# Kernel optimization log

Hardware: AMD Instinct MI355X
Metric: run time of the kernel (lower is better)

## Reference

```python
import jax, jax.numpy as jnp
import numpy as np

NUM_CLASSES = 21
THRESH = 0.5
NEGPOS = 3
VAR0, VAR1 = 0.1, 0.2
FEAT = 19
N_ANCH = 9
B = 256
NUM_OBJS = 12
P = FEAT * FEAT * N_ANCH  # 3249


def make_priors():
    # 19x19 grid, 3 scales x 3 aspect ratios (1, 2, 1/2) -> 9 anchors/cell, center form
    cxy = (np.arange(FEAT, dtype=np.float32) + 0.5) / FEAT
    cx, cy = np.meshgrid(cxy, cxy, indexing='ij')  # [19,19]
    scales = np.array([0.1, 0.2, 0.35], dtype=np.float32)
    ratios = np.array([1.0, 2.0, 0.5], dtype=np.float32)
    w = (scales[:, None] * np.sqrt(ratios)[None, :]).reshape(-1)  # [9]
    h = (scales[:, None] / np.sqrt(ratios)[None, :]).reshape(-1)
    cx = np.broadcast_to(cx[:, :, None], (FEAT, FEAT, N_ANCH))
    cy = np.broadcast_to(cy[:, :, None], (FEAT, FEAT, N_ANCH))
    w = np.broadcast_to(w[None, None, :], (FEAT, FEAT, N_ANCH))
    h = np.broadcast_to(h[None, None, :], (FEAT, FEAT, N_ANCH))
    pri = np.stack([cx, cy, w, h], axis=-1).reshape(-1, 4)
    return jnp.asarray(np.clip(pri, 1e-3, 1.0))


def setup_inputs() -> dict:
    key = jax.random.key(0)
    k1, k2, k3, k4, k5 = jax.random.split(key, 5)
    loc_data = jax.random.normal(k1, (B, P, 4), dtype=jnp.float32)
    conf_data = jax.random.normal(k2, (B, P, NUM_CLASSES), dtype=jnp.float32)
    priors = make_priors()
    xy = jax.random.uniform(k3, (B, NUM_OBJS, 2), minval=0.05, maxval=0.65)
    wh = jax.random.uniform(k4, (B, NUM_OBJS, 2), minval=0.05, maxval=0.30)
    labels = jax.random.randint(k5, (B, NUM_OBJS), 0, NUM_CLASSES - 1).astype(jnp.float32)
    targets = jnp.concatenate([xy, xy + wh, labels[..., None]], axis=-1)  # [B,O,5]
    return {"loc_data": loc_data, "conf_data": conf_data, "priors": priors, "targets": targets}


def point_form(boxes):  # (cx,cy,w,h) -> (x1,y1,x2,y2)
    return jnp.concatenate([boxes[:, :2] - boxes[:, 2:] / 2,
                            boxes[:, :2] + boxes[:, 2:] / 2], axis=1)


def jaccard(a, b):  # a: [n,4], b: [m,4] point form -> [n,m]
    lt = jnp.maximum(a[:, None, :2], b[None, :, :2])
    rb = jnp.minimum(a[:, None, 2:], b[None, :, 2:])
    inter = jnp.prod(jnp.clip(rb - lt, 0.0, None), axis=-1)
    area_a = jnp.prod(a[:, 2:] - a[:, :2], axis=-1)
    area_b = jnp.prod(b[:, 2:] - b[:, :2], axis=-1)
    return inter / (area_a[:, None] + area_b[None, :] - inter)


def encode(matched, priors):  # matched point-form [P,4], priors center-form [P,4]
    g_cxcy = ((matched[:, :2] + matched[:, 2:]) / 2 - priors[:, :2]) / (VAR0 * priors[:, 2:])
    g_wh = jnp.log((matched[:, 2:] - matched[:, :2]) / priors[:, 2:]) / VAR1
    return jnp.concatenate([g_cxcy, g_wh], axis=1)


def match_one(truths, labels, priors, priors_pt):
    overlaps = jaccard(truths, priors_pt)          # [O,P]
    best_prior_idx = jnp.argmax(overlaps, axis=1)  # [O]
    best_truth_ov = jnp.max(overlaps, axis=0)      # [P]
    best_truth_idx = jnp.argmax(overlaps, axis=0)  # [P]
    best_truth_ov = best_truth_ov.at[best_prior_idx].set(2.0)
    best_truth_idx = best_truth_idx.at[best_prior_idx].set(jnp.arange(truths.shape[0]))
    matches = truths[best_truth_idx]               # [P,4]
    conf = labels[best_truth_idx] + 1
    conf = jnp.where(best_truth_ov < THRESH, 0, conf)
    return encode(matches, priors), conf


def reference(loc_data, conf_data, priors, targets):
    truths = targets[:, :, :4]
    labels = targets[:, :, 4].astype(jnp.int32)
    priors_pt = point_form(priors)
    loc_t, conf_t = jax.vmap(lambda t, l: match_one(t, l, priors, priors_pt))(truths, labels)
    loc_t = jax.lax.stop_gradient(loc_t)
    conf_t = jax.lax.stop_gradient(conf_t)

    pos = conf_t > 0                                               # [B,P]
    # smooth L1 (sum) over matched priors
    d = loc_data - loc_t
    ad = jnp.abs(d)
    sl1 = jnp.where(ad < 1.0, 0.5 * d * d, ad - 0.5)
    loss_l = jnp.sum(sl1 * pos[..., None].astype(sl1.dtype))

    # per-prior CE = logsumexp - logit[target]
    lse = jax.nn.logsumexp(conf_data, axis=-1)                     # [B,P]
    gathered = jnp.take_along_axis(conf_data, conf_t[..., None], axis=2)[..., 0]
    ce = lse - gathered                                            # [B,P]

    # hard negative mining: double argsort rank of neg losses
    loss_c_mine = jnp.where(pos, 0.0, ce)
    loss_idx = jnp.argsort(-loss_c_mine, axis=1)
    idx_rank = jnp.argsort(loss_idx, axis=1)
    num_pos = jnp.sum(pos, axis=1, keepdims=True)                  # [B,1]
    num_neg = jnp.minimum(NEGPOS * num_pos, P - 1)
    neg = idx_rank < num_neg

    sel = pos | neg
    loss_c = jnp.sum(jnp.where(sel, ce, 0.0))

    have_centerloss = jnp.max(sel.reshape(B, FEAT, FEAT, N_ANCH), axis=3).reshape(-1)
    conf_t_featuremap = jnp.max(conf_t.reshape(B, FEAT, FEAT, N_ANCH), axis=3).reshape(-1)

    N = jnp.sum(num_pos).astype(loc_data.dtype)
    return loss_l / N, loss_c / N, conf_t_featuremap, have_centerloss
```

## Files before the change

### kernel.cpp

```cpp
#include <hip/hip_runtime.h>
#include <math.h>

#pragma clang fp contract(off)

#define BB      256
#define PP      3249
#define NCLS    21
#define NOBJ    12
#define CELLS   361
#define THRESH_ 0.5f
#define HB      4096

typedef float vf4 __attribute__((ext_vector_type(4), aligned(4)));


struct Row { vf4 a, b, c, d, e; float f; };

__device__ __forceinline__ Row load_row(const float* cd) {
    const vf4* q = (const vf4*)cd;
    Row r;
    r.a = q[0]; r.b = q[1]; r.c = q[2]; r.d = q[3]; r.e = q[4];
    r.f = cd[20];
    return r;
}

__device__ __forceinline__ float lse21(const Row& r) {
    float m = r.a[0];
    m = fmaxf(m, r.a[1]); m = fmaxf(m, r.a[2]); m = fmaxf(m, r.a[3]);
    m = fmaxf(m, r.b[0]); m = fmaxf(m, r.b[1]); m = fmaxf(m, r.b[2]); m = fmaxf(m, r.b[3]);
    m = fmaxf(m, r.c[0]); m = fmaxf(m, r.c[1]); m = fmaxf(m, r.c[2]); m = fmaxf(m, r.c[3]);
    m = fmaxf(m, r.d[0]); m = fmaxf(m, r.d[1]); m = fmaxf(m, r.d[2]); m = fmaxf(m, r.d[3]);
    m = fmaxf(m, r.e[0]); m = fmaxf(m, r.e[1]); m = fmaxf(m, r.e[2]); m = fmaxf(m, r.e[3]);
    m = fmaxf(m, r.f);
    float s = 0.0f;
    s += expf(r.a[0]-m); s += expf(r.a[1]-m); s += expf(r.a[2]-m); s += expf(r.a[3]-m);
    s += expf(r.b[0]-m); s += expf(r.b[1]-m); s += expf(r.b[2]-m); s += expf(r.b[3]-m);
    s += expf(r.c[0]-m); s += expf(r.c[1]-m); s += expf(r.c[2]-m); s += expf(r.c[3]-m);
    s += expf(r.d[0]-m); s += expf(r.d[1]-m); s += expf(r.d[2]-m); s += expf(r.d[3]-m);
    s += expf(r.e[0]-m); s += expf(r.e[1]-m); s += expf(r.e[2]-m); s += expf(r.e[3]-m);
    s += expf(r.f-m);
    return logf(s) + m;
}

template <int NBITS>
__device__ __forceinline__ void scan_hist(const unsigned* key_arr, int* hist,
                                          unsigned prefix, unsigned pmask,
                                          int shift, int tid, int lane) {
    for (int i = tid; i < PP; i += 1024) {
        unsigned key = key_arr[i];
        bool active = ((key & pmask) == prefix);
        unsigned bin = (key >> shift) & ((1u << NBITS) - 1u);
        unsigned long long mm = __ballot(active);
#pragma unroll
        for (int bit = 0; bit < NBITS; ++bit) {
            unsigned long long bb = __ballot(active && ((bin >> bit) & 1));
            mm &= ((bin >> bit) & 1) ? bb : ~bb;
        }
        if (active && (__ffsll((unsigned long long)mm) - 1 == lane))
            atomicAdd(&hist[bin], (int)__popcll(mm));
    }
}

__device__ __forceinline__ void pick_bin(const int* hist, int nbins, int kv, int lane,
                                         int* s_chosen, int* s_knext, int* s_cnt) {
    const int per = nbins >> 6;
    const int base = lane * per;
    int ls = 0;
    for (int k = 0; k < per; ++k) ls += hist[base + k];
    int x = ls;
#pragma unroll
    for (int off = 1; off < 64; off <<= 1) {
        int y = __shfl_down(x, off);
        if (lane + off < 64) x += y;
    }
    int cum = x - ls;
    for (int k = per - 1; k >= 0; --k) {
        int h = hist[base + k];
        if (cum < kv && kv <= cum + h) { *s_chosen = base + k; *s_knext = kv - cum; *s_cnt = h; }
        cum += h;
    }
}

__global__ __launch_bounds__(1024, 4) void fused_kernel(
    const float* __restrict__ loc, const float* __restrict__ conf,
    const float* __restrict__ priors, const float* __restrict__ targets,
    int* __restrict__ numpos, double* __restrict__ lossl,
    double* __restrict__ lossc, float* __restrict__ out)
{
    const int b = blockIdx.x, tid = threadIdx.x;
    const int lane = tid & 63, wid = tid >> 6;

    __shared__ float s_tx1[NOBJ], s_ty1[NOBJ], s_tx2[NOBJ], s_ty2[NOBJ];
    __shared__ float s_area_t[NOBJ];
    __shared__ int   s_label[NOBJ];
    __shared__ float s_bov[PP];
    __shared__ short s_bidx[PP];
    __shared__ float s_lse[PP];
    __shared__ float s_c0[PP];
    __shared__ unsigned s_key[PP];
    __shared__ unsigned char s_ct[PP];
    __shared__ int   s_bpi[NOBJ];
    __shared__ float s_wov[NOBJ][16];
    __shared__ int   s_widx[NOBJ][16];
    __shared__ int s_hist[2][HB];
    __shared__ int s_chosen, s_knext, s_cnt, s_nneg;
    __shared__ unsigned s_f;
    __shared__ double s_pl[16];
    __shared__ int    s_pn[16];
    __shared__ double s_pc[16];

    if (tid < NOBJ) {
        const float* t = targets + ((size_t)b * NOBJ + tid) * 5;
        float x1 = t[0], y1 = t[1], x2 = t[2], y2 = t[3];
        s_tx1[tid] = x1; s_ty1[tid] = y1; s_tx2[tid] = x2; s_ty2[tid] = y2;
        s_label[tid] = (int)t[4];
        s_area_t[tid] = (x2 - x1) * (y2 - y1);
    }
    __syncthreads();

    const float* confb = conf + (size_t)b * PP * NCLS;
    const int p0 = tid, p1 = tid + 1024, p2 = tid + 2048, p3 = tid + 3072;
    const bool h3 = (p3 < PP);

    vf4 pr0 = *(const vf4*)(priors + 4 * p0);
    vf4 pr1 = *(const vf4*)(priors + 4 * p1);
    vf4 pr2 = *(const vf4*)(priors + 4 * p2);
    vf4 pr3; if (h3) pr3 = *(const vf4*)(priors + 4 * p3);
    Row ra = load_row(confb + (size_t)p0 * NCLS);

    float l_bov[NOBJ];
    int   l_bidx[NOBJ];
#pragma unroll
    for (int j = 0; j < NOBJ; ++j) { l_bov[j] = -1.0f; l_bidx[j] = 0x7FFFFFFF; }

    auto iou_body = [&](vf4 prr, int p) {
        float cx = prr[0], cy = prr[1], w = prr[2], h = prr[3];
        float px1 = cx - w / 2.0f, py1 = cy - h / 2.0f;
        float px2 = cx + w / 2.0f, py2 = cy + h / 2.0f;
        float area_p = (px2 - px1) * (py2 - py1);
        float bov = -1.0f; int bidx = 0;
#pragma unroll
        for (int j = 0; j < NOBJ; ++j) {
            float ltx = fmaxf(s_tx1[j], px1);
            float lty = fmaxf(s_ty1[j], py1);
            float rbx = fminf(s_tx2[j], px2);
            float rby = fminf(s_ty2[j], py2);
            float iw = fmaxf(rbx - ltx, 0.0f);
            float ih = fmaxf(rby - lty, 0.0f);
            float inter = iw * ih;
            float iou = inter / ((s_area_t[j] + area_p) - inter);
            if (iou > bov) { bov = iou; bidx = j; }
            if (iou > l_bov[j]) { l_bov[j] = iou; l_bidx[j] = p; }
        }
        s_bov[p] = bov;
        s_bidx[p] = (short)bidx;
    };
    iou_body(pr0, p0);
    iou_body(pr1, p1);
    iou_body(pr2, p2);
    if (h3) iou_body(pr3, p3);

#pragma unroll
    for (int j = 0; j < NOBJ; ++j) {
        float ov = l_bov[j]; int ix = l_bidx[j];
#pragma unroll
        for (int off = 32; off > 0; off >>= 1) {
            float ov2 = __shfl_xor(ov, off);
            int   ix2 = __shfl_xor(ix, off);
            if (ov2 > ov || (ov2 == ov && ix2 < ix)) { ov = ov2; ix = ix2; }
        }
        if (lane == 0) { s_wov[j][wid] = ov; s_widx[j][wid] = ix; }
    }

    {
        Row rb = load_row(confb + (size_t)p1 * NCLS);
        s_lse[p0] = lse21(ra); s_c0[p0] = ra.a[0];
        Row rc = load_row(confb + (size_t)p2 * NCLS);
        s_lse[p1] = lse21(rb); s_c0[p1] = rb.a[0];
        Row rd; if (h3) rd = load_row(confb + (size_t)p3 * NCLS);
        s_lse[p2] = lse21(rc); s_c0[p2] = rc.a[0];
        if (h3) { s_lse[p3] = lse21(rd); s_c0[p3] = rd.a[0]; }
    }
    __syncthreads();

    if (tid < NOBJ) {
        float ov = s_wov[tid][0]; int ix = s_widx[tid][0];
#pragma unroll
        for (int w2 = 1; w2 < 16; ++w2) {
            float ov2 = s_wov[tid][w2]; int ix2 = s_widx[tid][w2];
            if (ov2 > ov || (ov2 == ov && ix2 < ix)) { ov = ov2; ix = ix2; }
        }
        s_bpi[tid] = ix;
    }
    __syncthreads();

    int bpi[NOBJ];
#pragma unroll
    for (int j = 0; j < NOBJ; ++j) bpi[j] = s_bpi[j];

    int my_pos = 0;
    double my_lossl = 0.0;
    for (int p = tid; p < PP; p += 1024) {
        int jov = -1;
#pragma unroll
        for (int j = 0; j < NOBJ; ++j) if (bpi[j] == p) jov = j;
        int idx; float ov;
        if (jov >= 0) { idx = jov; ov = 2.0f; }
        else          { idx = (int)s_bidx[p]; ov = s_bov[p]; }
        int c = (ov < THRESH_) ? 0 : (s_label[idx] + 1);
        s_ct[p] = (unsigned char)c;

        float lse = s_lse[p];
        float cdc = (c == 0) ? s_c0[p] : confb[(size_t)p * NCLS + c];
        float ce  = lse - cdc;

        float v = (c > 0) ? 0.0f : ce;
        s_key[p] = __float_as_uint(v);
        s_bov[p] = ce;

        if (c > 0) {
            ++my_pos;
            float cx = priors[4*p+0], cy = priors[4*p+1], w = priors[4*p+2], h = priors[4*p+3];
            float m0 = s_tx1[idx], m1 = s_ty1[idx], m2 = s_tx2[idx], m3 = s_ty2[idx];
            float g0 = ((m0 + m2) / 2.0f - cx) / (0.1f * w);
            float g1 = ((m1 + m3) / 2.0f - cy) / (0.1f * h);
            float g2 = logf((m2 - m0) / w) / 0.2f;
            float g3 = logf((m3 - m1) / h) / 0.2f;
            const float* ld = loc + ((size_t)b * PP + p) * 4;
            float d0 = ld[0] - g0, d1 = ld[1] - g1, d2 = ld[2] - g2, d3 = ld[3] - g3;
            float a0 = fabsf(d0), a1 = fabsf(d1), a2 = fabsf(d2), a3 = fabsf(d3);
            my_lossl += (double)((a0 < 1.0f) ? 0.5f * d0 * d0 : a0 - 0.5f);
            my_lossl += (double)((a1 < 1.0f) ? 0.5f * d1 * d1 : a1 - 0.5f);
            my_lossl += (double)((a2 < 1.0f) ? 0.5f * d2 * d2 : a2 - 0.5f);
            my_lossl += (double)((a3 < 1.0f) ? 0.5f * d3 * d3 : a3 - 0.5f);
        }
    }
#pragma unroll
    for (int off = 32; off > 0; off >>= 1) {
        my_lossl += __shfl_down(my_lossl, off);
        my_pos   += __shfl_down(my_pos, off);
    }
    if (lane == 0) { s_pl[wid] = my_lossl; s_pn[wid] = my_pos; }
    for (int k = tid; k < 2 * HB; k += 1024) ((int*)s_hist)[k] = 0;
    __syncthreads();

    unsigned prefix = 0u, pmask = 0u, fstar = 0u;
    int ptie = 0x7FFFFFFF;
    bool resolved = false;

    if (tid == 0) {
        double L = 0.0; int n = 0;
#pragma unroll
        for (int w2 = 0; w2 < 16; ++w2) { L += s_pl[w2]; n += s_pn[w2]; }
        lossl[b] = L; numpos[b] = n;
        s_nneg = min(3 * n, PP - 1);
    }
    scan_hist<12>(s_key, s_hist[0], 0u, 0u, 20, tid, lane);
    __syncthreads();
    if (tid < 64) pick_bin(s_hist[0], HB, s_nneg, lane, &s_chosen, &s_knext, &s_cnt);
    else { for (int k = tid - 64; k < HB; k += 960) s_hist[1][k] = 0; }
    __syncthreads();
    prefix = ((unsigned)s_chosen) << 20; pmask = 0xFFF00000u;
    if (s_cnt == 1) {
        for (int i = tid; i < PP; i += 1024) {
            unsigned key = s_key[i];
            if ((key & pmask) == prefix) s_f = key;
        }
        __syncthreads();
        fstar = s_f; resolved = true;
    }

    if (!resolved) {
        scan_hist<12>(s_key, s_hist[1], prefix, pmask, 8, tid, lane);
        __syncthreads();
        if (tid < 64) pick_bin(s_hist[1], HB, s_knext, lane, &s_chosen, &s_knext, &s_cnt);
        else { for (int k = tid - 64; k < HB; k += 960) s_hist[0][k] = 0; }
        __syncthreads();
        prefix |= ((unsigned)s_chosen) << 8; pmask |= 0x000FFF00u;
        if (s_cnt == 1) {
            for (int i = tid; i < PP; i += 1024) {
                unsigned key = s_key[i];
                if ((key & pmask) == prefix) s_f = key;
            }
            __syncthreads();
            fstar = s_f; resolved = true;
        }
    }

    if (!resolved) {
        scan_hist<8>(s_key, s_hist[0], prefix, pmask, 0, tid, lane);
        __syncthreads();
        if (tid < 64) pick_bin(s_hist[0], 256, s_knext, lane, &s_chosen, &s_knext, &s_cnt);
        else { for (int k = tid - 64; k < HB; k += 960) s_hist[1][k] = 0; }
        __syncthreads();
        prefix |= (unsigned)s_chosen;
        fstar = prefix;
        if (s_knext < s_cnt) {
            int* hist = s_hist[1];
            for (int i = tid; i < PP; i += 1024) {
                bool active = (s_key[i] == fstar);
                unsigned bin = 4095u - (unsigned)i;
                unsigned long long mm = __ballot(active);
#pragma unroll
                for (int bit = 0; bit < 12; ++bit) {
                    unsigned long long bb = __ballot(active && ((bin >> bit) & 1));
                    mm &= ((bin >> bit) & 1) ? bb : ~bb;
                }
                if (active && (__ffsll((unsigned long long)mm) - 1 == lane))
                    atomicAdd(&hist[bin], (int)__popcll(mm));
            }
            __syncthreads();
            if (tid < 64) pick_bin(hist, HB, s_knext, lane, &s_chosen, &s_knext, &s_cnt);
            __syncthreads();
            ptie = 4095 - s_chosen;
        }
    }

    double my_c = 0.0;
    for (int cI = tid; cI < CELLS; cI += 1024) {
        int mc = 0, hv = 0;
#pragma unroll
        for (int a = 0; a < 9; ++a) {
            int p = cI * 9 + a;
            int cv = s_ct[p];
            unsigned v = s_key[p];
            bool sel = (cv > 0) || (v > fstar) || (v == fstar && p <= ptie);
            mc = (cv > mc) ? cv : mc;
            hv |= sel ? 1 : 0;
            if (sel) my_c += (double)s_bov[p];
        }
        out[2 + (size_t)b * CELLS + cI] = (float)mc;
        out[2 + (size_t)BB * CELLS + (size_t)b * CELLS + cI] = (float)hv;
    }

#pragma unroll
    for (int off = 32; off > 0; off >>= 1) my_c += __shfl_down(my_c, off);
    if (lane == 0) s_pc[wid] = my_c;
    __syncthreads();
    if (tid == 0) {
        double L = 0.0;
#pragma unroll
        for (int w2 = 0; w2 < 16; ++w2) L += s_pc[w2];
        lossc[b] = L;
    }
}

__global__ __launch_bounds__(256) void finalize_kernel(
    const int* __restrict__ numpos, const double* __restrict__ lossl,
    const double* __restrict__ lossc, float* __restrict__ out)
{
    __shared__ double s_l[256], s_c[256];
    __shared__ int s_n[256];
    int tid = threadIdx.x;
    s_n[tid] = numpos[tid];
    s_l[tid] = lossl[tid];
    s_c[tid] = lossc[tid];
    __syncthreads();
    for (int s = 128; s > 0; s >>= 1) {
        if (tid < s) { s_n[tid] += s_n[tid + s]; s_l[tid] += s_l[tid + s]; s_c[tid] += s_c[tid + s]; }
        __syncthreads();
    }
    if (tid == 0) {
        double N = (double)s_n[0];
        out[0] = (float)(s_l[0] / N);
        out[1] = (float)(s_c[0] / N);
    }
}

extern "C" void kernel_launch(void* const* d_in, const int* in_sizes, int n_in,
                              void* d_out, int out_size, void* d_ws, size_t ws_size,
                              hipStream_t stream) {
    const float* loc     = (const float*)d_in[0];
    const float* conf    = (const float*)d_in[1];
    const float* priors  = (const float*)d_in[2];
    const float* targets = (const float*)d_in[3];
    float* out = (float*)d_out;

    double* ws_lossl  = (double*)d_ws;
    double* ws_lossc  = ws_lossl + BB;
    int*    ws_numpos = (int*)(ws_lossc + BB);

    hipLaunchKernelGGL(fused_kernel, dim3(BB), dim3(1024), 0, stream,
                       loc, conf, priors, targets, ws_numpos, ws_lossl, ws_lossc, out);
    hipLaunchKernelGGL(finalize_kernel, dim3(1), dim3(256), 0, stream,
                       ws_numpos, ws_lossl, ws_lossc, out);
}
```

Before: 141.9 us.

## Split IoU/logsumexp into a wide prep kernel and use 8-bit radix select

Moves the per-prior IoU matching and logsumexp over the 21 class logits into a separate prep kernel launched over 13 chunks per batch. This gives the memory-heavy conf read many more, smaller blocks than the original 256 large blocks. Per-object best-prior results are packed into 64-bit keys (IoU, inverted index) and reduced across chunks in the select kernel. The hard-negative radix select changes from 12-bit histograms (4096 bins) to four 8-bit passes plus a two-level tie-break, which shrinks the shared-memory footprint. The cost is an extra launch and a round trip of the per-prior records through global memory.

Measured after the change: 142.7 us. About the same (+0.5%).

```diff
diff --git a/kernel.cpp b/kernel.cpp
--- a/kernel.cpp
+++ b/kernel.cpp
@@ -8,10 +8,11 @@
 #define NCLS    21
 #define NOBJ    12
 #define CELLS   361
+#define CH      13
 #define THRESH_ 0.5f
-#define HB      4096
 
 typedef float vf4 __attribute__((ext_vector_type(4), aligned(4)));
+typedef float vrec __attribute__((ext_vector_type(4)));
 
 
 struct Row { vf4 a, b, c, d, e; float f; };
@@ -43,30 +44,24 @@
 }
 
 template <int NBITS>
-__device__ __forceinline__ void scan_hist(const unsigned* key_arr, int* hist,
-                                          unsigned prefix, unsigned pmask,
-                                          int shift, int tid, int lane) {
-    for (int i = tid; i < PP; i += 1024) {
-        unsigned key = key_arr[i];
-        bool active = ((key & pmask) == prefix);
-        unsigned bin = (key >> shift) & ((1u << NBITS) - 1u);
-        unsigned long long mm = __ballot(active);
-#pragma unroll
-        for (int bit = 0; bit < NBITS; ++bit) {
-            unsigned long long bb = __ballot(active && ((bin >> bit) & 1));
-            mm &= ((bin >> bit) & 1) ? bb : ~bb;
-        }
-        if (active && (__ffsll((unsigned long long)mm) - 1 == lane))
-            atomicAdd(&hist[bin], (int)__popcll(mm));
-    }
+__device__ __forceinline__ void agg_add(int* hist, bool active, unsigned bin, int lane) {
+    unsigned long long mm = __ballot(active);
+#pragma unroll
+    for (int bit = 0; bit < NBITS; ++bit) {
+        unsigned long long bb = __ballot(active && ((bin >> bit) & 1));
+        mm &= ((bin >> bit) & 1) ? bb : ~bb;
+    }
+    if (active && (__ffsll(mm) - 1 == lane))
+        atomicAdd(&hist[bin], (int)__popcll(mm));
 }
 
 __device__ __forceinline__ void pick_bin(const int* hist, int nbins, int kv, int lane,
                                          int* s_chosen, int* s_knext, int* s_cnt) {
-    const int per = nbins >> 6;
+    const int per = (nbins >= 64) ? (nbins >> 6) : 1;
     const int base = lane * per;
     int ls = 0;
-    for (int k = 0; k < per; ++k) ls += hist[base + k];
+    if (base < nbins)
+        for (int k = 0; k < per; ++k) ls += hist[base + k];
     int x = ls;
 #pragma unroll
     for (int off = 1; off < 64; off <<= 1) {
@@ -74,16 +69,85 @@
         if (lane + off < 64) x += y;
     }
     int cum = x - ls;
-    for (int k = per - 1; k >= 0; --k) {
-        int h = hist[base + k];
-        if (cum < kv && kv <= cum + h) { *s_chosen = base + k; *s_knext = kv - cum; *s_cnt = h; }
-        cum += h;
-    }
-}
-
-__global__ __launch_bounds__(1024, 4) void fused_kernel(
+    if (base < nbins) {
+        for (int k = per - 1; k >= 0; --k) {
+            int h = hist[base + k];
+            if (cum < kv && kv <= cum + h) { *s_chosen = base + k; *s_knext = kv - cum; *s_cnt = h; }
+            cum += h;
+        }
+    }
+}
+
+__global__ __launch_bounds__(256, 6) void prep_kernel(
+    const float* __restrict__ conf, const float* __restrict__ priors,
+    const float* __restrict__ targets, vrec* __restrict__ recs,
+    unsigned long long* __restrict__ pt)
+{
+    const int chunk = blockIdx.x, b = blockIdx.y;
+    const int tid = threadIdx.x, lane = tid & 63, wid = tid >> 6;
+    const int p = chunk * 256 + tid;
+    const bool valid = (p < PP);
+
+    __shared__ float s_tx1[NOBJ], s_ty1[NOBJ], s_tx2[NOBJ], s_ty2[NOBJ], s_area[NOBJ];
+    __shared__ unsigned long long s_wk[NOBJ][4];
+
+    if (tid < NOBJ) {
+        const float* t = targets + ((size_t)b * NOBJ + tid) * 5;
+        float x1 = t[0], y1 = t[1], x2 = t[2], y2 = t[3];
+        s_tx1[tid] = x1; s_ty1[tid] = y1; s_tx2[tid] = x2; s_ty2[tid] = y2;
+        s_area[tid] = (x2 - x1) * (y2 - y1);
+    }
+    __syncthreads();
+
+    vf4 pr = {0.0f, 0.0f, 0.0f, 0.0f};
+    if (valid) pr = *(const vf4*)(priors + 4 * p);
+    float px1 = pr[0] - pr[2] / 2.0f, py1 = pr[1] - pr[3] / 2.0f;
+    float px2 = pr[0] + pr[2] / 2.0f, py2 = pr[1] + pr[3] / 2.0f;
+    float area_p = (px2 - px1) * (py2 - py1);
+
+    float bov = -1.0f; int bidx = 0;
+#pragma unroll
+    for (int j = 0; j < NOBJ; ++j) {
+        float ltx = fmaxf(s_tx1[j], px1);
+        float lty = fmaxf(s_ty1[j], py1);
+        float rbx = fminf(s_tx2[j], px2);
+        float rby = fminf(s_ty2[j], py2);
+        float iw = fmaxf(rbx - ltx, 0.0f);
+        float ih = fmaxf(rby - lty, 0.0f);
+        float inter = iw * ih;
+        float iou = inter / ((s_area[j] + area_p) - inter);
+        if (iou > bov) { bov = iou; bidx = j; }
+        unsigned long long k = valid
+            ? (((unsigned long long)__float_as_uint(iou) << 32) | (0xFFFFFFFFu - (unsigned)p))
+            : 0ull;
+#pragma unroll
+        for (int off = 32; off > 0; off >>= 1) {
+            unsigned long long k2 = __shfl_xor(k, off);
+            if (k2 > k) k = k2;
+        }
+        if (lane == 0) s_wk[j][wid] = k;
+    }
+
+    if (valid) {
+        Row r = load_row(conf + ((size_t)b * PP + p) * NCLS);
+        float lse = lse21(r);
+        vrec rec;
+        rec[0] = bov; rec[1] = __int_as_float(bidx); rec[2] = lse; rec[3] = r.a[0];
+        recs[(size_t)b * PP + p] = rec;
+    }
+    __syncthreads();
+    if (tid < NOBJ) {
+        unsigned long long m = s_wk[tid][0];
+#pragma unroll
+        for (int w2 = 1; w2 < 4; ++w2) { unsigned long long v = s_wk[tid][w2]; if (v > m) m = v; }
+        pt[((size_t)b * CH + chunk) * NOBJ + tid] = m;
+    }
+}
+
+__global__ __launch_bounds__(1024, 4) void select_kernel(
     const float* __restrict__ loc, const float* __restrict__ conf,
     const float* __restrict__ priors, const float* __restrict__ targets,
+    const vrec* __restrict__ recs, const unsigned long long* __restrict__ pt,
     int* __restrict__ numpos, double* __restrict__ lossl,
     double* __restrict__ lossc, float* __restrict__ out)
 {
@@ -91,107 +155,37 @@
     const int lane = tid & 63, wid = tid >> 6;
 
     __shared__ float s_tx1[NOBJ], s_ty1[NOBJ], s_tx2[NOBJ], s_ty2[NOBJ];
-    __shared__ float s_area_t[NOBJ];
-    __shared__ int   s_label[NOBJ];
-    __shared__ float s_bov[PP];
-    __shared__ short s_bidx[PP];
-    __shared__ float s_lse[PP];
-    __shared__ float s_c0[PP];
+    __shared__ int   s_label[NOBJ], s_bpi[NOBJ];
     __shared__ unsigned s_key[PP];
+    __shared__ float s_ce[PP];
     __shared__ unsigned char s_ct[PP];
-    __shared__ int   s_bpi[NOBJ];
-    __shared__ float s_wov[NOBJ][16];
-    __shared__ int   s_widx[NOBJ][16];
-    __shared__ int s_hist[2][HB];
+    __shared__ int s_hist[2][256];
     __shared__ int s_chosen, s_knext, s_cnt, s_nneg;
-    __shared__ unsigned s_f;
     __shared__ double s_pl[16];
     __shared__ int    s_pn[16];
     __shared__ double s_pc[16];
 
+    const vrec* rb = recs + (size_t)b * PP;
+    vrec r0 = rb[tid];
+    vrec r1 = rb[tid + 1024];
+    vrec r2 = rb[tid + 2048];
+    const bool h3 = (tid + 3072 < PP);
+    vrec r3; if (h3) r3 = rb[tid + 3072];
+
     if (tid < NOBJ) {
         const float* t = targets + ((size_t)b * NOBJ + tid) * 5;
-        float x1 = t[0], y1 = t[1], x2 = t[2], y2 = t[3];
-        s_tx1[tid] = x1; s_ty1[tid] = y1; s_tx2[tid] = x2; s_ty2[tid] = y2;
+        s_tx1[tid] = t[0]; s_ty1[tid] = t[1]; s_tx2[tid] = t[2]; s_ty2[tid] = t[3];
         s_label[tid] = (int)t[4];
-        s_area_t[tid] = (x2 - x1) * (y2 - y1);
-    }
-    __syncthreads();
-
-    const float* confb = conf + (size_t)b * PP * NCLS;
-    const int p0 = tid, p1 = tid + 1024, p2 = tid + 2048, p3 = tid + 3072;
-    const bool h3 = (p3 < PP);
-
-    vf4 pr0 = *(const vf4*)(priors + 4 * p0);
-    vf4 pr1 = *(const vf4*)(priors + 4 * p1);
-    vf4 pr2 = *(const vf4*)(priors + 4 * p2);
-    vf4 pr3; if (h3) pr3 = *(const vf4*)(priors + 4 * p3);
-    Row ra = load_row(confb + (size_t)p0 * NCLS);
-
-    float l_bov[NOBJ];
-    int   l_bidx[NOBJ];
-#pragma unroll
-    for (int j = 0; j < NOBJ; ++j) { l_bov[j] = -1.0f; l_bidx[j] = 0x7FFFFFFF; }
-
-    auto iou_body = [&](vf4 prr, int p) {
-        float cx = prr[0], cy = prr[1], w = prr[2], h = prr[3];
-        float px1 = cx - w / 2.0f, py1 = cy - h / 2.0f;
-        float px2 = cx + w / 2.0f, py2 = cy + h / 2.0f;
-        float area_p = (px2 - px1) * (py2 - py1);
-        float bov = -1.0f; int bidx = 0;
-#pragma unroll
-        for (int j = 0; j < NOBJ; ++j) {
-            float ltx = fmaxf(s_tx1[j], px1);
-            float lty = fmaxf(s_ty1[j], py1);
-            float rbx = fminf(s_tx2[j], px2);
-            float rby = fminf(s_ty2[j], py2);
-            float iw = fmaxf(rbx - ltx, 0.0f);
-            float ih = fmaxf(rby - lty, 0.0f);
-            float inter = iw * ih;
-            float iou = inter / ((s_area_t[j] + area_p) - inter);
-            if (iou > bov) { bov = iou; bidx = j; }
-            if (iou > l_bov[j]) { l_bov[j] = iou; l_bidx[j] = p; }
-        }
-        s_bov[p] = bov;
-        s_bidx[p] = (short)bidx;
-    };
-    iou_body(pr0, p0);
-    iou_body(pr1, p1);
-    iou_body(pr2, p2);
-    if (h3) iou_body(pr3, p3);
-
-#pragma unroll
-    for (int j = 0; j < NOBJ; ++j) {
-        float ov = l_bov[j]; int ix = l_bidx[j];
-#pragma unroll
-        for (int off = 32; off > 0; off >>= 1) {
-            float ov2 = __shfl_xor(ov, off);
-            int   ix2 = __shfl_xor(ix, off);
-            if (ov2 > ov || (ov2 == ov && ix2 < ix)) { ov = ov2; ix = ix2; }
-        }
-        if (lane == 0) { s_wov[j][wid] = ov; s_widx[j][wid] = ix; }
-    }
-
-    {
-        Row rb = load_row(confb + (size_t)p1 * NCLS);
-        s_lse[p0] = lse21(ra); s_c0[p0] = ra.a[0];
-        Row rc = load_row(confb + (size_t)p2 * NCLS);
-        s_lse[p1] = lse21(rb); s_c0[p1] = rb.a[0];
-        Row rd; if (h3) rd = load_row(confb + (size_t)p3 * NCLS);
-        s_lse[p2] = lse21(rc); s_c0[p2] = rc.a[0];
-        if (h3) { s_lse[p3] = lse21(rd); s_c0[p3] = rd.a[0]; }
-    }
-    __syncthreads();
-
-    if (tid < NOBJ) {
-        float ov = s_wov[tid][0]; int ix = s_widx[tid][0];
-#pragma unroll
-        for (int w2 = 1; w2 < 16; ++w2) {
-            float ov2 = s_wov[tid][w2]; int ix2 = s_widx[tid][w2];
-            if (ov2 > ov || (ov2 == ov && ix2 < ix)) { ov = ov2; ix = ix2; }
-        }
-        s_bpi[tid] = ix;
-    }
+        const unsigned long long* q = pt + (size_t)b * CH * NOBJ + tid;
+        unsigned long long m = q[0];
+#pragma unroll
+        for (int c2 = 1; c2 < CH; ++c2) {
+            unsigned long long v = q[(size_t)c2 * NOBJ];
+            if (v > m) m = v;
+        }
+        s_bpi[tid] = (int)(0xFFFFFFFFu - (unsigned)(m & 0xFFFFFFFFull));
+    }
+    for (int k = tid; k < 512; k += 1024) ((int*)s_hist)[k] = 0;
     __syncthreads();
 
     int bpi[NOBJ];
@@ -200,32 +194,34 @@
 
     int my_pos = 0;
     double my_lossl = 0.0;
-    for (int p = tid; p < PP; p += 1024) {
+    const float* confb = conf + (size_t)b * PP * NCLS;
+
+    auto body = [&](vrec r, int p) {
+        float bov = r[0]; int bidx = __float_as_int(r[1]);
+        float lse = r[2]; float c0 = r[3];
         int jov = -1;
 #pragma unroll
         for (int j = 0; j < NOBJ; ++j) if (bpi[j] == p) jov = j;
         int idx; float ov;
         if (jov >= 0) { idx = jov; ov = 2.0f; }
-        else          { idx = (int)s_bidx[p]; ov = s_bov[p]; }
+        else          { idx = bidx; ov = bov; }
         int c = (ov < THRESH_) ? 0 : (s_label[idx] + 1);
         s_ct[p] = (unsigned char)c;
 
-        float lse = s_lse[p];
-        float cdc = (c == 0) ? s_c0[p] : confb[(size_t)p * NCLS + c];
+        float cdc = (c == 0) ? c0 : confb[(size_t)p * NCLS + c];
         float ce  = lse - cdc;
-
+        s_ce[p] = ce;
         float v = (c > 0) ? 0.0f : ce;
         s_key[p] = __float_as_uint(v);
-        s_bov[p] = ce;
 
         if (c > 0) {
             ++my_pos;
-            float cx = priors[4*p+0], cy = priors[4*p+1], w = priors[4*p+2], h = priors[4*p+3];
+            vf4 prr = *(const vf4*)(priors + 4 * p);
             float m0 = s_tx1[idx], m1 = s_ty1[idx], m2 = s_tx2[idx], m3 = s_ty2[idx];
-            float g0 = ((m0 + m2) / 2.0f - cx) / (0.1f * w);
-            float g1 = ((m1 + m3) / 2.0f - cy) / (0.1f * h);
-            float g2 = logf((m2 - m0) / w) / 0.2f;
-            float g3 = logf((m3 - m1) / h) / 0.2f;
+            float g0 = ((m0 + m2) / 2.0f - prr[0]) / (0.1f * prr[2]);
+            float g1 = ((m1 + m3) / 2.0f - prr[1]) / (0.1f * prr[3]);
+            float g2 = logf((m2 - m0) / prr[2]) / 0.2f;
+            float g3 = logf((m3 - m1) / prr[3]) / 0.2f;
             const float* ld = loc + ((size_t)b * PP + p) * 4;
             float d0 = ld[0] - g0, d1 = ld[1] - g1, d2 = ld[2] - g2, d3 = ld[3] - g3;
             float a0 = fabsf(d0), a1 = fabsf(d1), a2 = fabsf(d2), a3 = fabsf(d3);
@@ -234,20 +230,17 @@
             my_lossl += (double)((a2 < 1.0f) ? 0.5f * d2 * d2 : a2 - 0.5f);
             my_lossl += (double)((a3 < 1.0f) ? 0.5f * d3 * d3 : a3 - 0.5f);
         }
-    }
+    };
+    body(r0, tid); body(r1, tid + 1024); body(r2, tid + 2048);
+    if (h3) body(r3, tid + 3072);
+
 #pragma unroll
     for (int off = 32; off > 0; off >>= 1) {
         my_lossl += __shfl_down(my_lossl, off);
         my_pos   += __shfl_down(my_pos, off);
     }
     if (lane == 0) { s_pl[wid] = my_lossl; s_pn[wid] = my_pos; }
-    for (int k = tid; k < 2 * HB; k += 1024) ((int*)s_hist)[k] = 0;
-    __syncthreads();
-
-    unsigned prefix = 0u, pmask = 0u, fstar = 0u;
-    int ptie = 0x7FFFFFFF;
-    bool resolved = false;
-
+    __syncthreads();
     if (tid == 0) {
         double L = 0.0; int n = 0;
 #pragma unroll
@@ -255,65 +248,50 @@
         lossl[b] = L; numpos[b] = n;
         s_nneg = min(3 * n, PP - 1);
     }
-    scan_hist<12>(s_key, s_hist[0], 0u, 0u, 20, tid, lane);
-    __syncthreads();
-    if (tid < 64) pick_bin(s_hist[0], HB, s_nneg, lane, &s_chosen, &s_knext, &s_cnt);
-    else { for (int k = tid - 64; k < HB; k += 960) s_hist[1][k] = 0; }
-    __syncthreads();
-    prefix = ((unsigned)s_chosen) << 20; pmask = 0xFFF00000u;
-    if (s_cnt == 1) {
-        for (int i = tid; i < PP; i += 1024) {
-            unsigned key = s_key[i];
-            if ((key & pmask) == prefix) s_f = key;
-        }
-        __syncthreads();
-        fstar = s_f; resolved = true;
-    }
-
-    if (!resolved) {
-        scan_hist<12>(s_key, s_hist[1], prefix, pmask, 8, tid, lane);
-        __syncthreads();
-        if (tid < 64) pick_bin(s_hist[1], HB, s_knext, lane, &s_chosen, &s_knext, &s_cnt);
-        else { for (int k = tid - 64; k < HB; k += 960) s_hist[0][k] = 0; }
-        __syncthreads();
-        prefix |= ((unsigned)s_chosen) << 8; pmask |= 0x000FFF00u;
-        if (s_cnt == 1) {
+
+    unsigned prefix = 0u, pmask = 0u;
+    int ptie = 0x7FFFFFFF;
+    bool done = false;
+    const int shifts[4] = {24, 16, 8, 0};
+#pragma unroll
+    for (int r = 0; r < 4; ++r) {
+        if (!done) {
+            const int sh = shifts[r];
+            int* hist = s_hist[r & 1];
             for (int i = tid; i < PP; i += 1024) {
                 unsigned key = s_key[i];
-                if ((key & pmask) == prefix) s_f = key;
+                agg_add<8>(hist, (key & pmask) == prefix, (key >> sh) & 0xFFu, lane);
             }
             __syncthreads();
-            fstar = s_f; resolved = true;
-        }
-    }
-
-    if (!resolved) {
-        scan_hist<8>(s_key, s_hist[0], prefix, pmask, 0, tid, lane);
-        __syncthreads();
-        if (tid < 64) pick_bin(s_hist[0], 256, s_knext, lane, &s_chosen, &s_knext, &s_cnt);
-        else { for (int k = tid - 64; k < HB; k += 960) s_hist[1][k] = 0; }
-        __syncthreads();
-        prefix |= (unsigned)s_chosen;
-        fstar = prefix;
-        if (s_knext < s_cnt) {
-            int* hist = s_hist[1];
-            for (int i = tid; i < PP; i += 1024) {
-                bool active = (s_key[i] == fstar);
-                unsigned bin = 4095u - (unsigned)i;
-                unsigned long long mm = __ballot(active);
-#pragma unroll
-                for (int bit = 0; bit < 12; ++bit) {
-                    unsigned long long bb = __ballot(active && ((bin >> bit) & 1));
-                    mm &= ((bin >> bit) & 1) ? bb : ~bb;
-                }
-                if (active && (__ffsll((unsigned long long)mm) - 1 == lane))
-                    atomicAdd(&hist[bin], (int)__popcll(mm));
-            }
+            if (tid < 64) pick_bin(hist, 256, (r == 0) ? s_nneg : s_knext, lane,
+                                   &s_chosen, &s_knext, &s_cnt);
+            else { for (int k = tid - 64; k < 256; k += 960) s_hist[(r + 1) & 1][k] = 0; }
             __syncthreads();
-            if (tid < 64) pick_bin(hist, HB, s_knext, lane, &s_chosen, &s_knext, &s_cnt);
-            __syncthreads();
-            ptie = 4095 - s_chosen;
-        }
+            prefix |= ((unsigned)s_chosen) << sh;
+            pmask  |= 0xFFu << sh;
+            if (s_cnt == 1) done = true;
+        }
+    }
+
+    if (!done && s_knext < s_cnt) {
+        int* hist = s_hist[0];
+        for (int i = tid; i < PP; i += 1024)
+            agg_add<8>(hist, s_key[i] == prefix, ((4095u - (unsigned)i) >> 4) & 0xFFu, lane);
+        __syncthreads();
+        if (tid < 64) pick_bin(hist, 256, s_knext, lane, &s_chosen, &s_knext, &s_cnt);
+        else { for (int k = tid - 64; k < 256; k += 960) s_hist[1][k] = 0; }
+        __syncthreads();
+        const int binA = s_chosen;
+        int* hist2 = s_hist[1];
+        for (int i = tid; i < PP; i += 1024) {
+            unsigned hi = 4095u - (unsigned)i;
+            agg_add<4>(hist2, (s_key[i] == prefix) && (((hi >> 4) & 0xFFu) == (unsigned)binA),
+                       hi & 0xFu, lane);
+        }
+        __syncthreads();
+        if (tid < 64) pick_bin(hist2, 16, s_knext, lane, &s_chosen, &s_knext, &s_cnt);
+        __syncthreads();
+        ptie = 4095 - ((binA << 4) | s_chosen);
     }
 
     double my_c = 0.0;
@@ -323,11 +301,11 @@
         for (int a = 0; a < 9; ++a) {
             int p = cI * 9 + a;
             int cv = s_ct[p];
-            unsigned v = s_key[p];
-            bool sel = (cv > 0) || (v > fstar) || (v == fstar && p <= ptie);
+            unsigned km = s_key[p] & pmask;
+            bool sel = (cv > 0) || (km > prefix) || (km == prefix && p <= ptie);
             mc = (cv > mc) ? cv : mc;
             hv |= sel ? 1 : 0;
-            if (sel) my_c += (double)s_bov[p];
+            if (sel) my_c += (double)s_ce[p];
         }
         out[2 + (size_t)b * CELLS + cI] = (float)mc;
         out[2 + (size_t)BB * CELLS + (size_t)b * CELLS + cI] = (float)hv;
@@ -379,9 +357,14 @@
     double* ws_lossl  = (double*)d_ws;
     double* ws_lossc  = ws_lossl + BB;
     int*    ws_numpos = (int*)(ws_lossc + BB);
-
-    hipLaunchKernelGGL(fused_kernel, dim3(BB), dim3(1024), 0, stream,
-                       loc, conf, priors, targets, ws_numpos, ws_lossl, ws_lossc, out);
+    unsigned long long* ws_pt = (unsigned long long*)(ws_numpos + BB);
+    vrec*   ws_rec    = (vrec*)(ws_pt + (size_t)BB * CH * NOBJ);
+
+    hipLaunchKernelGGL(prep_kernel, dim3(CH, BB), dim3(256), 0, stream,
+                       conf, priors, targets, ws_rec, ws_pt);
+    hipLaunchKernelGGL(select_kernel, dim3(BB), dim3(1024), 0, stream,
+                       loc, conf, priors, targets, ws_rec, ws_pt,
+                       ws_numpos, ws_lossl, ws_lossc, out);
     hipLaunchKernelGGL(finalize_kernel, dim3(1), dim3(256), 0, stream,
                        ws_numpos, ws_lossl, ws_lossc, out);
 }
```
